# Kernel optimization log

Hardware: AMD Instinct MI355X
Metric: run time of the kernel (lower is better)

## Reference

```python
import jax, jax.numpy as jnp
import numpy as np

N_NODES = 50000
N_EDGES = 600000
IN_DIM = 128
HID_DIM = 512
OUT_DIM = 2


def setup_inputs() -> dict:
    key = jax.random.key(0)
    ks = jax.random.split(key, 8)
    x = jax.random.normal(ks[0], (N_NODES, IN_DIM), dtype=jnp.float32)
    edge_index = jax.random.randint(ks[1], (2, N_EDGES), 0, N_NODES, dtype=jnp.int32)
    s1 = 1.0 / np.sqrt(IN_DIM)
    s2 = 1.0 / np.sqrt(HID_DIM)
    # SAGEConv params: lin_l (applied to mean-aggregated neighbors, has bias),
    # lin_r (applied to root node features, no bias)
    W1l = jax.random.uniform(ks[2], (IN_DIM, HID_DIM), jnp.float32, -s1, s1)
    b1 = jax.random.uniform(ks[3], (HID_DIM,), jnp.float32, -s1, s1)
    W1r = jax.random.uniform(ks[4], (IN_DIM, HID_DIM), jnp.float32, -s1, s1)
    W2l = jax.random.uniform(ks[5], (HID_DIM, OUT_DIM), jnp.float32, -s2, s2)
    b2 = jax.random.uniform(ks[6], (OUT_DIM,), jnp.float32, -s2, s2)
    W2r = jax.random.uniform(ks[7], (HID_DIM, OUT_DIM), jnp.float32, -s2, s2)
    return {"x": x, "W1l": W1l, "b1": b1, "W1r": W1r,
            "W2l": W2l, "b2": b2, "W2r": W2r, "edge_index": edge_index}


def _sage_conv(x, edge_index, Wl, b, Wr):
    src, dst = edge_index[0], edge_index[1]
    msgs = x[src]                                             # [E, d]
    agg = jax.ops.segment_sum(msgs, dst, num_segments=x.shape[0])  # [N, d]
    deg = jax.ops.segment_sum(jnp.ones_like(dst, dtype=x.dtype), dst,
                              num_segments=x.shape[0])
    agg = agg / jnp.maximum(deg, 1.0)[:, None]                # mean aggregation
    return agg @ Wl + b + x @ Wr


def reference(x, W1l, b1, W1r, W2l, b2, W2r, edge_index):
    h = _sage_conv(x, edge_index, W1l, b1, W1r)
    h = jax.nn.relu(h)
    # dropout inactive (eval mode / force_dropout=False)
    out = _sage_conv(h, edge_index, W2l, b2, W2r)
    return jax.nn.log_softmax(out, axis=1)
```

## Files before the change

### kernel.cpp

```cpp
#include <hip/hip_runtime.h>
#include <math.h>
#include <stdint.h>

#define N_NODES 50000
#define N_EDGES 600000
#define IN_DIM 128
#define HID_DIM 512
#define M_PAD 50048
#define SCAN_NB 196

#define CASTX_NB 6250
#define DEG_NB   2344
#define CASTW_NB 544

typedef __bf16 bf16;
typedef __bf16 bf16x2 __attribute__((ext_vector_type(2)));
typedef __bf16 bf16x4 __attribute__((ext_vector_type(4)));
typedef __bf16 bf16x8 __attribute__((ext_vector_type(8)));
typedef float f32x4 __attribute__((ext_vector_type(4)));

#define GLDS(gp, lp) __builtin_amdgcn_global_load_lds( \
    (const __attribute__((address_space(1))) uint32_t*)(gp), \
    (__attribute__((address_space(3))) uint32_t*)(lp), 16, 0, 0)


__global__ __launch_bounds__(256) void prep_kernel(
    const float* __restrict__ x, bf16* __restrict__ xb,
    const int* __restrict__ dst, int* __restrict__ deg,
    const float* __restrict__ W1l, const float* __restrict__ W1r,
    const float* __restrict__ W2l, const float* __restrict__ W2r,
    bf16* __restrict__ Wt, bf16* __restrict__ W2bt) {
    int b = blockIdx.x;
    int t = threadIdx.x;
    if (b < CASTX_NB) {
        int i = b * 256 + t;
        float4 v = ((const float4*)x)[i];
        bf16x4 o = {(bf16)v.x, (bf16)v.y, (bf16)v.z, (bf16)v.w};
        *(bf16x4*)(xb + (size_t)i * 4) = o;
    } else if (b < CASTX_NB + DEG_NB) {
        int i = (b - CASTX_NB) * 256 + t;
        if (i < N_EDGES) atomicAdd(&deg[dst[i]], 1);
    } else {
        int idx = (b - CASTX_NB - DEG_NB) * 256 + t;
        if (idx < 512 * 256) {
            int n = idx >> 8;
            int k = idx & 255;
            float v = (k < IN_DIM) ? W1l[(size_t)k * HID_DIM + n]
                                   : W1r[(size_t)(k - IN_DIM) * HID_DIM + n];
            Wt[idx] = (bf16)v;
        } else {
            int j = idx - 512 * 256;
            int n = j >> 9;
            int k = j & 511;
            float v = 0.f;
            if (n == 0) v = W2l[k * 2 + 0];
            else if (n == 1) v = W2l[k * 2 + 1];
            else if (n == 2) v = W2r[k * 2 + 0];
            else if (n == 3) v = W2r[k * 2 + 1];
            W2bt[j] = (bf16)v;
        }
    }
}


__global__ __launch_bounds__(256) void scan1_kernel(const int* __restrict__ deg,
                                                    int* __restrict__ bsum) {
    int t = threadIdx.x;
    int i = blockIdx.x * 256 + t;
    int v = (i < N_NODES) ? deg[i] : 0;
#pragma unroll
    for (int m = 1; m < 64; m <<= 1) v += __shfl_xor(v, m);
    __shared__ int ws_[4];
    int w = t >> 6, l = t & 63;
    if (l == 0) ws_[w] = v;
    __syncthreads();
    if (t == 0) bsum[blockIdx.x] = ws_[0] + ws_[1] + ws_[2] + ws_[3];
}

__global__ __launch_bounds__(256) void scan3_kernel(const int* __restrict__ deg,
                                                    const int* __restrict__ bsum,
                                                    int* __restrict__ offsets,
                                                    int* __restrict__ cursor) {
    int t = threadIdx.x;
    int blk = blockIdx.x;
    int i = blk * 256 + t;
    int l = t & 63, w = t >> 6;
    int v = (i < N_NODES) ? deg[i] : 0;
    int inc = v;
#pragma unroll
    for (int off = 1; off < 64; off <<= 1) {
        int y = __shfl_up(inc, off);
        if (l >= off) inc += y;
    }
    __shared__ int wsum[4];
    __shared__ int lookback;
    if (l == 63) wsum[w] = inc;
    __syncthreads();
    if (t < 64) {
        int s = 0;
        for (int u = t; u < blk; u += 64) s += bsum[u];
#pragma unroll
        for (int m = 1; m < 64; m <<= 1) s += __shfl_xor(s, m);
        if (t == 0) lookback = s;
    }
    __syncthreads();
    int add = lookback;
    for (int u = 0; u < w; ++u) add += wsum[u];
    int ex = add + inc - v;
    if (i < N_NODES) { offsets[i] = ex; cursor[i] = ex; }
    if (blk == 0 && t == 0) offsets[N_NODES] = N_EDGES;
}

__global__ void csr_fill_kernel(const int* __restrict__ src, const int* __restrict__ dst,
                                int* __restrict__ cursor, int* __restrict__ csr_src) {
    int i = blockIdx.x * blockDim.x + threadIdx.x;
    if (i < N_EDGES) {
        int p = atomicAdd(&cursor[dst[i]], 1);
        csr_src[p] = src[i];
    }
}


__global__ __launch_bounds__(256) void agg1_kernel(
    const bf16* __restrict__ xb, const int* __restrict__ offsets,
    const int* __restrict__ csr_src, bf16* __restrict__ agg1b) {
    int t = threadIdx.x;
    int w = t >> 6, l = t & 63;
    int g = l >> 4;
    int sl = l & 15;
    int n = blockIdx.x * 16 + w * 4 + g;
    int s0 = offsets[n], s1 = offsets[n + 1];
    float a[8] = {};
    int e = s0;
    for (; e + 4 <= s1; e += 4) {
        int i0 = csr_src[e + 0];
        int i1 = csr_src[e + 1];
        int i2 = csr_src[e + 2];
        int i3 = csr_src[e + 3];
        bf16x8 v0 = *(const bf16x8*)(xb + (size_t)i0 * IN_DIM + sl * 8);
        bf16x8 v1 = *(const bf16x8*)(xb + (size_t)i1 * IN_DIM + sl * 8);
        bf16x8 v2 = *(const bf16x8*)(xb + (size_t)i2 * IN_DIM + sl * 8);
        bf16x8 v3 = *(const bf16x8*)(xb + (size_t)i3 * IN_DIM + sl * 8);
#pragma unroll
        for (int u = 0; u < 8; ++u)
            a[u] += (float)v0[u] + (float)v1[u] + (float)v2[u] + (float)v3[u];
    }
    for (; e < s1; ++e) {
        int i0 = csr_src[e];
        bf16x8 v0 = *(const bf16x8*)(xb + (size_t)i0 * IN_DIM + sl * 8);
#pragma unroll
        for (int u = 0; u < 8; ++u) a[u] += (float)v0[u];
    }
    float inv = 1.0f / fmaxf((float)(s1 - s0), 1.0f);
    bf16x8 o;
#pragma unroll
    for (int u = 0; u < 8; ++u) o[u] = (bf16)(a[u] * inv);
    *(bf16x8*)(agg1b + (size_t)n * IN_DIM + sl * 8) = o;
}


__global__ __launch_bounds__(256) void gemm1_kernel(
    const bf16* __restrict__ agg1b, const bf16* __restrict__ xb,
    const bf16* __restrict__ Wt, const float* __restrict__ b1,
    const bf16* __restrict__ W2bt, float* __restrict__ zpart) {
    __shared__ __align__(16) char smem[128 * 136 * 2];
    bf16 (*As)[128][32] = (bf16(*)[128][32])smem;
    bf16 (*Bs)[128][32] = (bf16(*)[128][32])(smem + 16384);
    bf16 (*Hs)[136] = (bf16(*)[136])smem;
    int tid = threadIdx.x;
    int w = tid >> 6;
    int lane = tid & 63;
    int q = lane >> 4, rr = lane & 15;
    int cb = blockIdx.x;
    int n0 = cb * 128;
    int row0 = blockIdx.y * 128;
    int wm = (w & 1) * 64, wn = (w >> 1) * 64;
    int lr = lane >> 2;
    int lc = (lane & 3) * 8;

    auto stage = [&](int ki) {
        const bf16* Asrc;
        int kb;
        if (ki < 4) { Asrc = agg1b; kb = ki * 32; }
        else        { Asrc = xb;    kb = ki * 32 - IN_DIM; }
        int kw = ki * 32;
        int buf = ki & 1;
#pragma unroll
        for (int j = 0; j < 2; ++j) {
            int r = w * 32 + j * 16 + lr;
            GLDS(Asrc + (size_t)(row0 + r) * IN_DIM + kb + lc,
                 &As[buf][w * 32 + j * 16][0]);
            GLDS(Wt + (size_t)(n0 + r) * 256 + kw + lc,
                 &Bs[buf][w * 32 + j * 16][0]);
        }
    };

    f32x4 acc[4][4] = {};
    stage(0);
#pragma unroll
    for (int ki = 0; ki < 8; ++ki) {
        __syncthreads();
        if (ki + 1 < 8) stage(ki + 1);
        int buf = ki & 1;
        bf16x8 af[4], bfr[4];
#pragma unroll
        for (int i = 0; i < 4; ++i)
            af[i] = *(const bf16x8*)&As[buf][wm + i * 16 + rr][q * 8];
#pragma unroll
        for (int j = 0; j < 4; ++j)
            bfr[j] = *(const bf16x8*)&Bs[buf][wn + j * 16 + rr][q * 8];
#pragma unroll
        for (int i = 0; i < 4; ++i)
#pragma unroll
            for (int j = 0; j < 4; ++j)
                acc[i][j] = __builtin_amdgcn_mfma_f32_16x16x32_bf16(
                    af[i], bfr[j], acc[i][j], 0, 0, 0);
    }
    __syncthreads();
    float bias[4];
#pragma unroll
    for (int j = 0; j < 4; ++j) bias[j] = b1[n0 + wn + j * 16 + rr];
#pragma unroll
    for (int i = 0; i < 4; ++i) {
#pragma unroll
        for (int rg = 0; rg < 4; ++rg) {
            int mrow = wm + i * 16 + q * 4 + rg;
#pragma unroll
            for (int j = 0; j < 4; ++j)
                Hs[mrow][wn + j * 16 + rr] =
                    (bf16)fmaxf(acc[i][j][rg] + bias[j], 0.f);
        }
    }
    __syncthreads();
    bf16x8 wf[4];
#pragma unroll
    for (int ks = 0; ks < 4; ++ks)
        wf[ks] = *(const bf16x8*)(W2bt + (size_t)rr * 512 + n0 + ks * 32 + q * 8);
    f32x4 zacc[2] = {};
#pragma unroll
    for (int mt = 0; mt < 2; ++mt)
#pragma unroll
        for (int ks = 0; ks < 4; ++ks) {
            bf16x8 afz = *(const bf16x8*)&Hs[w * 32 + mt * 16 + rr][ks * 32 + q * 8];
            zacc[mt] = __builtin_amdgcn_mfma_f32_16x16x32_bf16(
                afz, wf[ks], zacc[mt], 0, 0, 0);
        }
    if (rr < 4) {
#pragma unroll
        for (int mt = 0; mt < 2; ++mt)
#pragma unroll
            for (int rg = 0; rg < 4; ++rg) {
                int grow = row0 + w * 32 + mt * 16 + q * 4 + rg;
                zpart[(size_t)grow * 16 + cb * 4 + rr] = zacc[mt][rg];
            }
    }
}


__global__ __launch_bounds__(256) void zsum_kernel(const float* __restrict__ zpart,
                                                   float* __restrict__ z) {
    int n = blockIdx.x * blockDim.x + threadIdx.x;
    if (n >= N_NODES) return;
    const float4* p = (const float4*)(zpart + (size_t)n * 16);
    float4 a = p[0], b = p[1], c = p[2], d = p[3];
    float4 o = {a.x + b.x + c.x + d.x, a.y + b.y + c.y + d.y,
                a.z + b.z + c.z + d.z, a.w + b.w + c.w + d.w};
    *(float4*)(z + (size_t)n * 4) = o;
}


__global__ void final_kernel(const float* __restrict__ z, const int* __restrict__ offsets,
                             const int* __restrict__ csr_src, const float* __restrict__ b2,
                             float* __restrict__ out) {
    int n = blockIdx.x * blockDim.x + threadIdx.x;
    if (n >= N_NODES) return;
    int s0 = offsets[n], s1 = offsets[n + 1];
    float a0 = 0.f, a1 = 0.f;
    int e = s0;
    for (; e + 4 <= s1; e += 4) {
        int i0 = csr_src[e], i1 = csr_src[e + 1];
        int i2 = csr_src[e + 2], i3 = csr_src[e + 3];
        float2 v0 = *(const float2*)(z + (size_t)i0 * 4);
        float2 v1 = *(const float2*)(z + (size_t)i1 * 4);
        float2 v2 = *(const float2*)(z + (size_t)i2 * 4);
        float2 v3 = *(const float2*)(z + (size_t)i3 * 4);
        a0 += v0.x + v1.x + v2.x + v3.x;
        a1 += v0.y + v1.y + v2.y + v3.y;
    }
    for (; e < s1; ++e) {
        int s = csr_src[e];
        float2 v = *(const float2*)(z + (size_t)s * 4);
        a0 += v.x;
        a1 += v.y;
    }
    float inv = 1.0f / fmaxf((float)(s1 - s0), 1.0f);
    float2 zs = *(const float2*)(z + (size_t)n * 4 + 2);
    float o0 = a0 * inv + b2[0] + zs.x;
    float o1 = a1 * inv + b2[1] + zs.y;
    float m = fmaxf(o0, o1);
    float lse = logf(expf(o0 - m) + expf(o1 - m));
    float2 o = {o0 - m - lse, o1 - m - lse};
    *(float2*)(out + (size_t)n * 2) = o;
}


extern "C" void kernel_launch(void* const* d_in, const int* in_sizes, int n_in,
                              void* d_out, int out_size, void* d_ws, size_t ws_size,
                              hipStream_t stream) {
    const float* x   = (const float*)d_in[0];
    const float* W1l = (const float*)d_in[1];
    const float* b1  = (const float*)d_in[2];
    const float* W1r = (const float*)d_in[3];
    const float* W2l = (const float*)d_in[4];
    const float* b2  = (const float*)d_in[5];
    const float* W2r = (const float*)d_in[6];
    const int* edge  = (const int*)d_in[7];
    const int* src = edge;
    const int* dst = edge + N_EDGES;
    float* out = (float*)d_out;

    char* ws = (char*)d_ws;
    size_t off = 0;
    auto alloc = [&](size_t bytes) -> void* {
        void* p = ws + off;
        off += (bytes + 255) & ~(size_t)255;
        return p;
    };
    int* deg     = (int*)alloc((size_t)N_NODES * 4);
    int* offsets = (int*)alloc((size_t)(N_NODES + 1) * 4);
    int* cursor  = (int*)alloc((size_t)N_NODES * 4);
    int* csr_src = (int*)alloc((size_t)N_EDGES * 4);
    int* bsum    = (int*)alloc((size_t)SCAN_NB * 4);
    bf16* xb     = (bf16*)alloc((size_t)M_PAD * IN_DIM * 2);
    bf16* agg1b  = (bf16*)alloc((size_t)M_PAD * IN_DIM * 2);
    bf16* Wt     = (bf16*)alloc((size_t)HID_DIM * 256 * 2);
    bf16* W2bt   = (bf16*)alloc((size_t)16 * HID_DIM * 2);
    float* zpart = (float*)alloc((size_t)M_PAD * 16 * 4);
    float* z     = (float*)alloc((size_t)N_NODES * 4 * 4);

    hipMemsetAsync(deg, 0, (size_t)N_NODES * 4, stream);
    prep_kernel<<<CASTX_NB + DEG_NB + CASTW_NB, 256, 0, stream>>>(
        x, xb, dst, deg, W1l, W1r, W2l, W2r, Wt, W2bt);
    scan1_kernel<<<SCAN_NB, 256, 0, stream>>>(deg, bsum);
    scan3_kernel<<<SCAN_NB, 256, 0, stream>>>(deg, bsum, offsets, cursor);
    csr_fill_kernel<<<(N_EDGES + 255) / 256, 256, 0, stream>>>(src, dst, cursor, csr_src);
    agg1_kernel<<<N_NODES / 16, 256, 0, stream>>>(xb, offsets, csr_src, agg1b);
    gemm1_kernel<<<dim3(4, M_PAD / 128), 256, 0, stream>>>(
        agg1b, xb, Wt, b1, W2bt, zpart);
    zsum_kernel<<<(N_NODES + 255) / 256, 256, 0, stream>>>(zpart, z);
    final_kernel<<<(N_NODES + 255) / 256, 256, 0, stream>>>(z, offsets, csr_src, b2, out);
}
```

Baseline: 208.0 us.

## Build CSR via per-block LDS histograms instead of global atomics

```diff
diff --git a/kernel.cpp b/kernel.cpp
--- a/kernel.cpp
+++ b/kernel.cpp
@@ -10,8 +10,12 @@
 #define SCAN_NB 196
 
 #define CASTX_NB 6250
-#define DEG_NB   2344
 #define CASTW_NB 544
+
+#define NB_H 64
+#define CE4_H 2344
+#define NPAD 50048
+#define H2_WORDS 25024
 
 typedef __bf16 bf16;
 typedef __bf16 bf16x2 __attribute__((ext_vector_type(2)));
@@ -26,7 +30,6 @@
 
 __global__ __launch_bounds__(256) void prep_kernel(
     const float* __restrict__ x, bf16* __restrict__ xb,
-    const int* __restrict__ dst, int* __restrict__ deg,
     const float* __restrict__ W1l, const float* __restrict__ W1r,
     const float* __restrict__ W2l, const float* __restrict__ W2r,
     bf16* __restrict__ Wt, bf16* __restrict__ W2bt) {
@@ -37,11 +40,8 @@
         float4 v = ((const float4*)x)[i];
         bf16x4 o = {(bf16)v.x, (bf16)v.y, (bf16)v.z, (bf16)v.w};
         *(bf16x4*)(xb + (size_t)i * 4) = o;
-    } else if (b < CASTX_NB + DEG_NB) {
-        int i = (b - CASTX_NB) * 256 + t;
-        if (i < N_EDGES) atomicAdd(&deg[dst[i]], 1);
     } else {
-        int idx = (b - CASTX_NB - DEG_NB) * 256 + t;
+        int idx = (b - CASTX_NB) * 256 + t;
         if (idx < 512 * 256) {
             int n = idx >> 8;
             int k = idx & 255;
@@ -63,11 +63,43 @@
 }
 
 
-__global__ __launch_bounds__(256) void scan1_kernel(const int* __restrict__ deg,
-                                                    int* __restrict__ bsum) {
+__global__ __launch_bounds__(512) void hist_kernel(
+    const int* __restrict__ dst, uint32_t* __restrict__ Hg32) {
+    __shared__ uint32_t h2[H2_WORDS];
+    int b = blockIdx.x, t = threadIdx.x;
+    for (int j = t; j < H2_WORDS; j += 512) h2[j] = 0;
+    __syncthreads();
+    int e40 = b * CE4_H;
+    int e4end = min(e40 + CE4_H, N_EDGES / 4);
+    for (int e4 = e40 + t; e4 < e4end; e4 += 512) {
+        int4 d = ((const int4*)dst)[e4];
+        atomicAdd(&h2[d.x >> 1], 1u << ((d.x & 1) << 4));
+        atomicAdd(&h2[d.y >> 1], 1u << ((d.y & 1) << 4));
+        atomicAdd(&h2[d.z >> 1], 1u << ((d.z & 1) << 4));
+        atomicAdd(&h2[d.w >> 1], 1u << ((d.w & 1) << 4));
+    }
+    __syncthreads();
+    for (int j = t; j < H2_WORDS; j += 512)
+        Hg32[(size_t)b * H2_WORDS + j] = h2[j];
+}
+
+
+__global__ __launch_bounds__(256) void scancols_kernel(
+    const uint16_t* __restrict__ Hg, int* __restrict__ deg,
+    uint16_t* __restrict__ PB, int* __restrict__ bsum) {
     int t = threadIdx.x;
-    int i = blockIdx.x * 256 + t;
-    int v = (i < N_NODES) ? deg[i] : 0;
+    int n = blockIdx.x * 256 + t;
+    int running = 0;
+    if (n < NPAD) {
+#pragma unroll 4
+        for (int b = 0; b < NB_H; ++b) {
+            int v = Hg[(size_t)b * NPAD + n];
+            PB[(size_t)b * NPAD + n] = (uint16_t)running;
+            running += v;
+        }
+        deg[n] = running;
+    }
+    int v = (n < N_NODES) ? running : 0;
 #pragma unroll
     for (int m = 1; m < 64; m <<= 1) v += __shfl_xor(v, m);
     __shared__ int ws_[4];
@@ -79,8 +111,7 @@
 
 __global__ __launch_bounds__(256) void scan3_kernel(const int* __restrict__ deg,
                                                     const int* __restrict__ bsum,
-                                                    int* __restrict__ offsets,
-                                                    int* __restrict__ cursor) {
+                                                    int* __restrict__ offsets) {
     int t = threadIdx.x;
     int blk = blockIdx.x;
     int i = blk * 256 + t;
@@ -107,16 +138,39 @@
     int add = lookback;
     for (int u = 0; u < w; ++u) add += wsum[u];
     int ex = add + inc - v;
-    if (i < N_NODES) { offsets[i] = ex; cursor[i] = ex; }
+    if (i < N_NODES) offsets[i] = ex;
     if (blk == 0 && t == 0) offsets[N_NODES] = N_EDGES;
 }
 
-__global__ void csr_fill_kernel(const int* __restrict__ src, const int* __restrict__ dst,
-                                int* __restrict__ cursor, int* __restrict__ csr_src) {
-    int i = blockIdx.x * blockDim.x + threadIdx.x;
-    if (i < N_EDGES) {
-        int p = atomicAdd(&cursor[dst[i]], 1);
-        csr_src[p] = src[i];
+
+__global__ __launch_bounds__(512) void fill_kernel(
+    const int* __restrict__ src, const int* __restrict__ dst,
+    const int* __restrict__ offsets, const uint16_t* __restrict__ PB,
+    int* __restrict__ csr_src) {
+    __shared__ uint32_t h2[H2_WORDS];
+    int b = blockIdx.x, t = threadIdx.x;
+    for (int j = t; j < H2_WORDS; j += 512) h2[j] = 0;
+    __syncthreads();
+    const uint16_t* pb = PB + (size_t)b * NPAD;
+    int e40 = b * CE4_H;
+    int e4end = min(e40 + CE4_H, N_EDGES / 4);
+    for (int e4 = e40 + t; e4 < e4end; e4 += 512) {
+        int4 d = ((const int4*)dst)[e4];
+        int4 s = ((const int4*)src)[e4];
+        int sh0 = (d.x & 1) << 4, sh1 = (d.y & 1) << 4;
+        int sh2 = (d.z & 1) << 4, sh3 = (d.w & 1) << 4;
+        uint32_t r0 = atomicAdd(&h2[d.x >> 1], 1u << sh0);
+        uint32_t r1 = atomicAdd(&h2[d.y >> 1], 1u << sh1);
+        uint32_t r2 = atomicAdd(&h2[d.z >> 1], 1u << sh2);
+        uint32_t r3 = atomicAdd(&h2[d.w >> 1], 1u << sh3);
+        int k0 = (int)((r0 >> sh0) & 0xffff);
+        int k1 = (int)((r1 >> sh1) & 0xffff);
+        int k2 = (int)((r2 >> sh2) & 0xffff);
+        int k3 = (int)((r3 >> sh3) & 0xffff);
+        csr_src[offsets[d.x] + (int)pb[d.x] + k0] = s.x;
+        csr_src[offsets[d.y] + (int)pb[d.y] + k1] = s.y;
+        csr_src[offsets[d.z] + (int)pb[d.z] + k2] = s.z;
+        csr_src[offsets[d.w] + (int)pb[d.w] + k3] = s.w;
     }
 }
 
@@ -326,9 +380,8 @@
         off += (bytes + 255) & ~(size_t)255;
         return p;
     };
-    int* deg     = (int*)alloc((size_t)N_NODES * 4);
+    int* deg     = (int*)alloc((size_t)NPAD * 4);
     int* offsets = (int*)alloc((size_t)(N_NODES + 1) * 4);
-    int* cursor  = (int*)alloc((size_t)N_NODES * 4);
     int* csr_src = (int*)alloc((size_t)N_EDGES * 4);
     int* bsum    = (int*)alloc((size_t)SCAN_NB * 4);
     bf16* xb     = (bf16*)alloc((size_t)M_PAD * IN_DIM * 2);
@@ -338,12 +391,16 @@
     float* zpart = (float*)alloc((size_t)M_PAD * 16 * 4);
     float* z     = (float*)alloc((size_t)N_NODES * 4 * 4);
 
-    hipMemsetAsync(deg, 0, (size_t)N_NODES * 4, stream);
-    prep_kernel<<<CASTX_NB + DEG_NB + CASTW_NB, 256, 0, stream>>>(
-        x, xb, dst, deg, W1l, W1r, W2l, W2r, Wt, W2bt);
-    scan1_kernel<<<SCAN_NB, 256, 0, stream>>>(deg, bsum);
-    scan3_kernel<<<SCAN_NB, 256, 0, stream>>>(deg, bsum, offsets, cursor);
-    csr_fill_kernel<<<(N_EDGES + 255) / 256, 256, 0, stream>>>(src, dst, cursor, csr_src);
+    uint32_t* Hg32 = (uint32_t*)agg1b;
+    uint16_t* PB   = (uint16_t*)((char*)agg1b + (size_t)NB_H * H2_WORDS * 4);
+
+    prep_kernel<<<CASTX_NB + CASTW_NB, 256, 0, stream>>>(
+        x, xb, W1l, W1r, W2l, W2r, Wt, W2bt);
+    hist_kernel<<<NB_H, 512, 0, stream>>>(dst, Hg32);
+    scancols_kernel<<<SCAN_NB, 256, 0, stream>>>(
+        (const uint16_t*)Hg32, deg, PB, bsum);
+    scan3_kernel<<<SCAN_NB, 256, 0, stream>>>(deg, bsum, offsets);
+    fill_kernel<<<NB_H, 512, 0, stream>>>(src, dst, offsets, PB, csr_src);
     agg1_kernel<<<N_NODES / 16, 256, 0, stream>>>(xb, offsets, csr_src, agg1b);
     gemm1_kernel<<<dim3(4, M_PAD / 128), 256, 0, stream>>>(
         agg1b, xb, Wt, b1, W2bt, zpart);
```

Result: faster. 186.5 us (-10.3%).
